# Optimization experiments

Hardware: AMD Instinct MI355X
Metric: run time of the kernel (lower is better)

The kernel has to match this reference:

```python
import jax, jax.numpy as jnp
import numpy as np


def setup_inputs() -> dict:
    key = jax.random.key(0)
    k1, k2, k3, k4 = jax.random.split(key, 4)
    B, S, D, Y = 8, 2048, 512, 8921
    # xavier_uniform scale for [Y, D] weights
    lim = float(np.sqrt(6.0 / (Y + D)))
    x = jax.random.normal(k1, (B, S, D), dtype=jnp.float32)
    U_w = jax.random.uniform(k2, (Y, D), minval=-lim, maxval=lim, dtype=jnp.float32)
    final_w = jax.random.uniform(k3, (Y, D), minval=-lim, maxval=lim, dtype=jnp.float32)
    final_b = jax.random.normal(k4, (Y,), dtype=jnp.float32) * 0.02
    return {"x": x, "U_w": U_w, "final_w": final_w, "final_b": final_b}


def reference(x, U_w, final_w, final_b):
    # att: [B, Y, S] = U_w @ x^T
    att = jnp.einsum("yd,bsd->bys", U_w, x)
    alpha = jax.nn.softmax(att, axis=2)          # softmax over sequence
    m = jnp.einsum("bys,bsd->byd", alpha, x)      # per-label context [B, Y, D]
    y = jnp.einsum("yd,byd->by", final_w, m) + final_b  # [B, Y]
    return y
```

## Files before the change

### kernel.cpp

```cpp
#include <hip/hip_runtime.h>
#include <hip/hip_bf16.h>

constexpr int B_ = 8;
constexpr int S_ = 2048;
constexpr int D_ = 512;
constexpr int Y_ = 8921;
constexpr int MT_ = 70;
constexpr int SG_ = 4;

typedef __attribute__((ext_vector_type(8))) __bf16 bf16x8;
typedef __attribute__((ext_vector_type(4))) float f32x4;

__device__ __forceinline__ int swz_el(int row, int ksel8) {
  return row * 64 + ((ksel8 ^ row) & 7) * 8;
}

__global__ __launch_bounds__(256) void cvtW(const float* __restrict__ U,
                                            const float* __restrict__ F,
                                            __hip_bfloat16* __restrict__ wsW) {
  const int c = blockIdx.x * 256 + threadIdx.x;
  const int tile = c >> 11;
  const int row = (c >> 3) & 255;
  const int cs = c & 7;
  const int mt = tile >> 3, kt = tile & 7;
  const int ch = cs ^ (row & 7);
  const int g = row >> 5, h = (row >> 4) & 1, w = row & 15;
  const int y = mt * 128 + g * 16 + w;
  float4 f0 = {0.f, 0.f, 0.f, 0.f}, f1 = {0.f, 0.f, 0.f, 0.f};
  if (y < Y_) {
    const float* src = (h ? F : U) + (size_t)y * D_ + kt * 64 + ch * 8;
    f0 = reinterpret_cast<const float4*>(src)[0];
    f1 = reinterpret_cast<const float4*>(src)[1];
  }
  bf16x8 v;
  v[0] = (__bf16)f0.x; v[1] = (__bf16)f0.y; v[2] = (__bf16)f0.z; v[3] = (__bf16)f0.w;
  v[4] = (__bf16)f1.x; v[5] = (__bf16)f1.y; v[6] = (__bf16)f1.z; v[7] = (__bf16)f1.w;
  *reinterpret_cast<bf16x8*>(wsW + (size_t)c * 8) = v;
}

__global__ __launch_bounds__(256) void cvtX(const float* __restrict__ x,
                                            __hip_bfloat16* __restrict__ wsX) {
  const int c = blockIdx.x * 256 + threadIdx.x;
  const int lane = c & 63;
  const int idx2 = (c >> 6) & 7;
  const int wn = (c >> 9) & 3;
  const int kt = (c >> 11) & 7;
  const int st = (c >> 14) & 7;
  const int b = (c >> 17) & 7;
  const int n = idx2 >> 1, kk = idx2 & 1;
  const int s = st * 256 + wn * 64 + n * 16 + (lane & 15);
  const int k = kt * 64 + kk * 32 + (lane >> 4) * 8;
  const float* src = x + ((size_t)b * S_ + s) * D_ + k;
  const float4 f0 = reinterpret_cast<const float4*>(src)[0];
  const float4 f1 = reinterpret_cast<const float4*>(src)[1];
  bf16x8 v;
  v[0] = (__bf16)f0.x; v[1] = (__bf16)f0.y; v[2] = (__bf16)f0.z; v[3] = (__bf16)f0.w;
  v[4] = (__bf16)f1.x; v[5] = (__bf16)f1.y; v[6] = (__bf16)f1.z; v[7] = (__bf16)f1.w;
  *reinterpret_cast<bf16x8*>(wsX + (size_t)c * 8) = v;
}

__global__ __launch_bounds__(256) void zeroLN(float* __restrict__ LN, int n) {
  const int i = blockIdx.x * 256 + threadIdx.x;
  if (i < n) LN[i] = 0.f;
}

__global__ __launch_bounds__(256) void combine(const float* __restrict__ Lg,
                                               const float* __restrict__ Ng,
                                               const float* __restrict__ fb,
                                               float* __restrict__ out) {
  const int y = blockIdx.x * 256 + threadIdx.x;
  const int b = blockIdx.y;
  if (y < Y_) out[(size_t)b * Y_ + y] = Ng[b * Y_ + y] / Lg[b * Y_ + y] + fb[y];
}

typedef const __attribute__((address_space(1))) void gv_t;
typedef __attribute__((address_space(3))) void lv_t;

__device__ __forceinline__ void gld_lds16(const void* g, void* l) {
  __builtin_amdgcn_global_load_lds((gv_t*)g, (lv_t*)l, 16, 0, 0);
}

__global__ __launch_bounds__(512, 2) void pool_main(
    const __hip_bfloat16* __restrict__ wsW, const __hip_bfloat16* __restrict__ wsX,
    float* __restrict__ Lg, float* __restrict__ Ng) {
  const int bid = blockIdx.x;
  const int b = bid & 7;
  const int r = bid >> 3;
  const int mt = r % MT_;
  const int sg = r / MT_;

  const int tid = threadIdx.x;
  const int lane = tid & 63;
  const int wid = tid >> 6;
  const int wm = wid >> 2;
  const int wn = wid & 3;
  const int l15 = lane & 15;
  const int l4 = lane >> 4;

  extern __shared__ __bf16 ldsA[];
  float* redLN = reinterpret_cast<float*>(ldsA + 4 * 16384);
  float* redL = redLN;
  float* redN = redLN + 128;

  if (tid < 256) redLN[tid] = 0.f;

  const __bf16* Wbase = (const __bf16*)wsW + (size_t)mt * 8 * 16384;
  const __bf16* xc = (const __bf16*)wsX +
      ((size_t)(b * 8 + sg * 2) * 8) * 16384 + wn * 4096 + lane * 8;

  f32x4 acc[8][4];
  bf16x8 X0[4], X1[4];

  auto stageA = [&](int wkt, int buf) {
    const char* src = (const char*)(Wbase + wkt * 16384) + wid * 4096 + lane * 16;
    char* dst = (char*)ldsA + buf * 32768 + wid * 4096;
#pragma unroll
    for (int i = 0; i < 4; ++i)
      gld_lds16(src + i * 1024, dst + i * 1024);
  };

  auto fold = [&]() {
#pragma unroll
    for (int g = 0; g < 4; ++g)
#pragma unroll
      for (int q = 0; q < 4; ++q) {
        float l = 0.f, nn = 0.f;
#pragma unroll
        for (int n = 0; n < 4; ++n) {
          const float e = __expf(acc[2 * g][n][q]);
          l += e;
          nn = fmaf(e, acc[2 * g + 1][n][q], nn);
        }
#pragma unroll
        for (int mask = 1; mask <= 8; mask <<= 1) {
          l += __shfl_xor(l, mask);
          nn += __shfl_xor(nn, mask);
        }
        if (l15 == 0) {
          const int yl = wm * 64 + g * 16 + (l4 << 2) + q;
          atomicAdd(&redL[yl], l);
          atomicAdd(&redN[yl], nn);
        }
      }
  };

  auto zacc = [&]() {
#pragma unroll
    for (int m = 0; m < 8; ++m)
#pragma unroll
      for (int n = 0; n < 4; ++n) acc[m][n] = (f32x4){0.f, 0.f, 0.f, 0.f};
  };

  stageA(0, 0);
  stageA(1, 1);
  stageA(2, 2);
#pragma unroll
  for (int n = 0; n < 4; ++n)
    X0[n] = *reinterpret_cast<const bf16x8*>(xc + n * 1024);
  asm volatile("s_waitcnt vmcnt(0) lgkmcnt(0)" ::: "memory");
  __builtin_amdgcn_s_barrier();
  __builtin_amdgcn_sched_barrier(0);
  zacc();

  for (int t = 0; t < 16; ++t) {
    if (t == 8) { fold(); zacc(); }
    const __bf16* A = ldsA + (t & 3) * 16384;

    {
      bf16x8 af[4];
#pragma unroll
      for (int j = 0; j < 4; ++j)
        af[j] = *reinterpret_cast<const bf16x8*>(
            &A[swz_el(wm * 128 + j * 16 + l15, l4)]);
#pragma unroll
      for (int n = 0; n < 4; ++n)
        X1[n] = *reinterpret_cast<const bf16x8*>(xc + n * 1024 + 512);
      if (t <= 12) stageA((t + 3) & 7, (t + 3) & 3);
      __builtin_amdgcn_s_barrier();
      __builtin_amdgcn_s_setprio(1);
#pragma unroll
      for (int j = 0; j < 4; ++j)
#pragma unroll
        for (int n = 0; n < 4; ++n)
          acc[j][n] = __builtin_amdgcn_mfma_f32_16x16x32_bf16(af[j], X0[n], acc[j][n], 0, 0, 0);
      __builtin_amdgcn_s_setprio(0);
      __builtin_amdgcn_s_barrier();
    }
    {
      bf16x8 af[4];
#pragma unroll
      for (int j = 0; j < 4; ++j)
        af[j] = *reinterpret_cast<const bf16x8*>(
            &A[swz_el(wm * 128 + (4 + j) * 16 + l15, l4)]);
      __builtin_amdgcn_s_barrier();
      __builtin_amdgcn_s_setprio(1);
#pragma unroll
      for (int j = 0; j < 4; ++j)
#pragma unroll
        for (int n = 0; n < 4; ++n)
          acc[4 + j][n] = __builtin_amdgcn_mfma_f32_16x16x32_bf16(af[j], X0[n], acc[4 + j][n], 0, 0, 0);
      __builtin_amdgcn_s_setprio(0);
      __builtin_amdgcn_s_barrier();
    }
    {
      bf16x8 af[4];
#pragma unroll
      for (int j = 0; j < 4; ++j)
        af[j] = *reinterpret_cast<const bf16x8*>(
            &A[swz_el(wm * 128 + j * 16 + l15, 4 + l4)]);
      if (t < 15) {
#pragma unroll
        for (int n = 0; n < 4; ++n)
          X0[n] = *reinterpret_cast<const bf16x8*>(xc + 16384 + n * 1024);
      }
      __builtin_amdgcn_s_barrier();
      __builtin_amdgcn_s_setprio(1);
#pragma unroll
      for (int j = 0; j < 4; ++j)
#pragma unroll
        for (int n = 0; n < 4; ++n)
          acc[j][n] = __builtin_amdgcn_mfma_f32_16x16x32_bf16(af[j], X1[n], acc[j][n], 0, 0, 0);
      __builtin_amdgcn_s_setprio(0);
      __builtin_amdgcn_s_barrier();
    }
    {
      bf16x8 af[4];
#pragma unroll
      for (int j = 0; j < 4; ++j)
        af[j] = *reinterpret_cast<const bf16x8*>(
            &A[swz_el(wm * 128 + (4 + j) * 16 + l15, 4 + l4)]);
      __builtin_amdgcn_s_barrier();
      __builtin_amdgcn_s_setprio(1);
#pragma unroll
      for (int j = 0; j < 4; ++j)
#pragma unroll
        for (int n = 0; n < 4; ++n)
          acc[4 + j][n] = __builtin_amdgcn_mfma_f32_16x16x32_bf16(af[j], X1[n], acc[4 + j][n], 0, 0, 0);
      __builtin_amdgcn_s_setprio(0);
      asm volatile("s_waitcnt vmcnt(8)" ::: "memory");
      __builtin_amdgcn_s_barrier();
      __builtin_amdgcn_sched_barrier(0);
    }
    xc += 16384;
  }
  fold();

  __syncthreads();
  if (tid < 128) {
    const int y = mt * 128 + tid;
    if (y < Y_) {
      atomicAdd(&Lg[(size_t)b * Y_ + y], redL[tid]);
      atomicAdd(&Ng[(size_t)b * Y_ + y], redN[tid]);
    }
  }
}

constexpr int FB_BY = 128, FB_BS = 64, FB_BK = 64;

__device__ __forceinline__ int fswz(int row, int k) {
  return row * FB_BK + ((((k >> 3) ^ row) & 7) << 3) + (k & 7);
}

template <int CHUNKS>
__device__ __forceinline__ void fb_stage(const float* __restrict__ gbase, int rstride,
                                         int maxrow, __bf16* lds, int tid) {
#pragma unroll
  for (int i = 0; i < CHUNKS / 256; ++i) {
    const int c = tid + 256 * i;
    const int row = c >> 3;
    const int ch = c & 7;
    float4 f0 = {0.f, 0.f, 0.f, 0.f}, f1 = {0.f, 0.f, 0.f, 0.f};
    if (row < maxrow) {
      const float4* p = reinterpret_cast<const float4*>(gbase + (size_t)row * rstride + ch * 8);
      f0 = p[0]; f1 = p[1];
    }
    bf16x8 v;
    v[0] = (__bf16)f0.x; v[1] = (__bf16)f0.y; v[2] = (__bf16)f0.z; v[3] = (__bf16)f0.w;
    v[4] = (__bf16)f1.x; v[5] = (__bf16)f1.y; v[6] = (__bf16)f1.z; v[7] = (__bf16)f1.w;
    *reinterpret_cast<bf16x8*>(&lds[fswz(row, ch * 8)]) = v;
  }
}

__global__ __launch_bounds__(256) void output_layer_fallback(
    const float* __restrict__ x, const float* __restrict__ Uw,
    const float* __restrict__ Fw, const float* __restrict__ fb,
    float* __restrict__ out) {
  const int b = blockIdx.y;
  const int y0 = blockIdx.x * FB_BY;
  const int tid = threadIdx.x;
  const int lane = tid & 63;
  const int w = tid >> 6;
  const int wm = (w >> 1) * 64, wn = (w & 1) * 32;
  __shared__ __bf16 sU[FB_BY * FB_BK], sF[FB_BY * FB_BK], sX[FB_BS * FB_BK];
  float Ls[4][4], Ns[4][4];
#pragma unroll
  for (int m = 0; m < 4; ++m)
#pragma unroll
    for (int q = 0; q < 4; ++q) { Ls[m][q] = 0.f; Ns[m][q] = 0.f; }
  const float* xb = x + (size_t)b * S_ * D_;
  const int umax = Y_ - y0;
  for (int s0 = 0; s0 < S_; s0 += FB_BS) {
    f32x4 accA[4][2] = {}, accP[4][2] = {};
    for (int k0 = 0; k0 < D_; k0 += FB_BK) {
      __syncthreads();
      fb_stage<FB_BY * 8>(Uw + (size_t)y0 * D_ + k0, D_, umax, sU, tid);
      fb_stage<FB_BY * 8>(Fw + (size_t)y0 * D_ + k0, D_, umax, sF, tid);
      fb_stage<FB_BS * 8>(xb + (size_t)s0 * D_ + k0, D_, FB_BS, sX, tid);
      __syncthreads();
#pragma unroll
      for (int kk = 0; kk < 2; ++kk) {
        const int kb = kk * 32 + (lane >> 4) * 8;
        bf16x8 bx[2];
#pragma unroll
        for (int n = 0; n < 2; ++n)
          bx[n] = *reinterpret_cast<const bf16x8*>(&sX[fswz(wn + n * 16 + (lane & 15), kb)]);
#pragma unroll
        for (int m = 0; m < 4; ++m) {
          const bf16x8 aU = *reinterpret_cast<const bf16x8*>(&sU[fswz(wm + m * 16 + (lane & 15), kb)]);
          const bf16x8 aF = *reinterpret_cast<const bf16x8*>(&sF[fswz(wm + m * 16 + (lane & 15), kb)]);
#pragma unroll
          for (int n = 0; n < 2; ++n) {
            accA[m][n] = __builtin_amdgcn_mfma_f32_16x16x32_bf16(aU, bx[n], accA[m][n], 0, 0, 0);
            accP[m][n] = __builtin_amdgcn_mfma_f32_16x16x32_bf16(aF, bx[n], accP[m][n], 0, 0, 0);
          }
        }
      }
    }
#pragma unroll
    for (int m = 0; m < 4; ++m)
#pragma unroll
      for (int n = 0; n < 2; ++n)
#pragma unroll
        for (int q = 0; q < 4; ++q) {
          const float e = __expf(accA[m][n][q]);
          Ls[m][q] += e;
          Ns[m][q] = fmaf(e, accP[m][n][q], Ns[m][q]);
        }
  }
  __syncthreads();
  float* redL = reinterpret_cast<float*>(sU);
  float* redN = reinterpret_cast<float*>(sF);
  for (int i = tid; i < FB_BY; i += 256) { redL[i] = 0.f; redN[i] = 0.f; }
  __syncthreads();
#pragma unroll
  for (int m = 0; m < 4; ++m)
#pragma unroll
    for (int q = 0; q < 4; ++q) {
      float l = Ls[m][q], nn = Ns[m][q];
#pragma unroll
      for (int mask = 1; mask <= 8; mask <<= 1) {
        l += __shfl_xor(l, mask);
        nn += __shfl_xor(nn, mask);
      }
      if ((lane & 15) == 0) {
        const int yl = wm + m * 16 + ((lane >> 4) << 2) + q;
        atomicAdd(&redL[yl], l);
        atomicAdd(&redN[yl], nn);
      }
    }
  __syncthreads();
  for (int i = tid; i < FB_BY; i += 256) {
    const int y = y0 + i;
    if (y < Y_) out[(size_t)b * Y_ + y] = redN[i] / redL[i] + fb[y];
  }
}

extern "C" void kernel_launch(void* const* d_in, const int* in_sizes, int n_in,
                              void* d_out, int out_size, void* d_ws,
                              size_t ws_size, hipStream_t stream) {
  const float* x = (const float*)d_in[0];
  const float* Uw = (const float*)d_in[1];
  const float* Fw = (const float*)d_in[2];
  const float* fb = (const float*)d_in[3];
  float* out = (float*)d_out;

  constexpr size_t W_EL = (size_t)MT_ * 8 * 16384;
  constexpr size_t X_EL = (size_t)B_ * 64 * 16384;
  constexpr size_t LN_FL = (size_t)2 * B_ * Y_;
  constexpr size_t WS_NEED = (W_EL + X_EL) * 2 + LN_FL * 4;
  constexpr int LDS_BYTES = 4 * 32768 + 1024;

  if (ws_size >= WS_NEED) {
    __hip_bfloat16* wsW = (__hip_bfloat16*)d_ws;
    __hip_bfloat16* wsX = wsW + W_EL;
    float* Lg = (float*)(wsX + X_EL);
    float* Ng = Lg + (size_t)B_ * Y_;

    cvtW<<<dim3((unsigned)(W_EL / 8 / 256)), dim3(256), 0, stream>>>(Uw, Fw, wsW);
    cvtX<<<dim3((unsigned)(X_EL / 8 / 256)), dim3(256), 0, stream>>>(x, wsX);
    zeroLN<<<dim3((unsigned)((LN_FL + 255) / 256)), dim3(256), 0, stream>>>(Lg, (int)LN_FL);

    hipFuncSetAttribute((const void*)pool_main,
                        hipFuncAttributeMaxDynamicSharedMemorySize, LDS_BYTES);
    pool_main<<<dim3(MT_ * B_ * SG_), dim3(512), LDS_BYTES, stream>>>(wsW, wsX, Lg, Ng);
    combine<<<dim3((Y_ + 255) / 256, B_), dim3(256), 0, stream>>>(Lg, Ng, fb, out);
  } else {
    output_layer_fallback<<<dim3(MT_, B_), dim3(256), 0, stream>>>(x, Uw, Fw, fb, out);
  }
}
```

Measured before the change: 399.7 us.

## Stage X tiles through LDS with double-buffered combined W/X loads

The X pre-conversion kernel now writes x in the same swizzled 256x64 tile layout used for the weights. The main pooling loop then stages both the W and X tiles into LDS with direct global-to-LDS loads, double-buffered, instead of a 4-deep W ring plus per-wave register loads of X. Each iteration now does one __syncthreads and two 32-deep MFMA phases that read X fragments from LDS, replacing four barrier-separated sub-phases. This simplifies synchronisation and shares X loads across waves, but the prefetch distance drops from three tiles to one and X now adds LDS read traffic.

```diff
diff --git a/kernel.cpp b/kernel.cpp
--- a/kernel.cpp
+++ b/kernel.cpp
@@ -41,16 +41,13 @@
 __global__ __launch_bounds__(256) void cvtX(const float* __restrict__ x,
                                             __hip_bfloat16* __restrict__ wsX) {
   const int c = blockIdx.x * 256 + threadIdx.x;
-  const int lane = c & 63;
-  const int idx2 = (c >> 6) & 7;
-  const int wn = (c >> 9) & 3;
-  const int kt = (c >> 11) & 7;
-  const int st = (c >> 14) & 7;
-  const int b = (c >> 17) & 7;
-  const int n = idx2 >> 1, kk = idx2 & 1;
-  const int s = st * 256 + wn * 64 + n * 16 + (lane & 15);
-  const int k = kt * 64 + kk * 32 + (lane >> 4) * 8;
-  const float* src = x + ((size_t)b * S_ + s) * D_ + k;
+  const int tile = c >> 11;
+  const int row = (c >> 3) & 255;
+  const int cs = c & 7;
+  const int b = tile >> 6, st = (tile >> 3) & 7, kt = tile & 7;
+  const int ch = cs ^ (row & 7);
+  const int s = st * 256 + row;
+  const float* src = x + ((size_t)b * S_ + s) * D_ + kt * 64 + ch * 8;
   const float4 f0 = reinterpret_cast<const float4*>(src)[0];
   const float4 f1 = reinterpret_cast<const float4*>(src)[1];
   bf16x8 v;
@@ -98,25 +95,26 @@
   const int l4 = lane >> 4;
 
   extern __shared__ __bf16 ldsA[];
-  float* redLN = reinterpret_cast<float*>(ldsA + 4 * 16384);
-  float* redL = redLN;
-  float* redN = redLN + 128;
-
-  if (tid < 256) redLN[tid] = 0.f;
+  float* redL = reinterpret_cast<float*>(ldsA + 65536);
+  float* redN = redL + 128;
+
+  if (tid < 256) redL[tid] = 0.f;
 
   const __bf16* Wbase = (const __bf16*)wsW + (size_t)mt * 8 * 16384;
-  const __bf16* xc = (const __bf16*)wsX +
-      ((size_t)(b * 8 + sg * 2) * 8) * 16384 + wn * 4096 + lane * 8;
+  const __bf16* Xbase = (const __bf16*)wsX + ((size_t)(b * 8 + sg * 2) * 8) * 16384;
 
   f32x4 acc[8][4];
-  bf16x8 X0[4], X1[4];
-
-  auto stageA = [&](int wkt, int buf) {
-    const char* src = (const char*)(Wbase + wkt * 16384) + wid * 4096 + lane * 16;
-    char* dst = (char*)ldsA + buf * 32768 + wid * 4096;
-#pragma unroll
-    for (int i = 0; i < 4; ++i)
-      gld_lds16(src + i * 1024, dst + i * 1024);
+
+  auto stageBoth = [&](int t1) {
+    const int par = t1 & 1;
+    const char* srcW = (const char*)(Wbase + (t1 & 7) * 16384) + wid * 4096 + lane * 16;
+    const char* srcX = (const char*)(Xbase + (size_t)t1 * 16384) + wid * 4096 + lane * 16;
+    char* dstW = (char*)ldsA + par * 32768 + wid * 4096;
+    char* dstX = (char*)ldsA + 65536 + par * 32768 + wid * 4096;
+#pragma unroll
+    for (int i = 0; i < 4; ++i) gld_lds16(srcW + i * 1024, dstW + i * 1024);
+#pragma unroll
+    for (int i = 0; i < 4; ++i) gld_lds16(srcX + i * 1024, dstX + i * 1024);
   };
 
   auto fold = [&]() {
@@ -151,97 +149,50 @@
       for (int n = 0; n < 4; ++n) acc[m][n] = (f32x4){0.f, 0.f, 0.f, 0.f};
   };
 
-  stageA(0, 0);
-  stageA(1, 1);
-  stageA(2, 2);
-#pragma unroll
-  for (int n = 0; n < 4; ++n)
-    X0[n] = *reinterpret_cast<const bf16x8*>(xc + n * 1024);
-  asm volatile("s_waitcnt vmcnt(0) lgkmcnt(0)" ::: "memory");
-  __builtin_amdgcn_s_barrier();
-  __builtin_amdgcn_sched_barrier(0);
+  stageBoth(0);
   zacc();
 
   for (int t = 0; t < 16; ++t) {
-    if (t == 8) { fold(); zacc(); }
-    const __bf16* A = ldsA + (t & 3) * 16384;
+    __syncthreads();
+    if (t < 15) stageBoth(t + 1);
+
+    const __bf16* A = ldsA + (t & 1) * 16384;
+    const __bf16* Xl = ldsA + 32768 + (t & 1) * 16384;
 
     {
-      bf16x8 af[4];
-#pragma unroll
-      for (int j = 0; j < 4; ++j)
-        af[j] = *reinterpret_cast<const bf16x8*>(
-            &A[swz_el(wm * 128 + j * 16 + l15, l4)]);
+      bf16x8 xf[4], af[8];
 #pragma unroll
       for (int n = 0; n < 4; ++n)
-        X1[n] = *reinterpret_cast<const bf16x8*>(xc + n * 1024 + 512);
-      if (t <= 12) stageA((t + 3) & 7, (t + 3) & 3);
-      __builtin_amdgcn_s_barrier();
+        xf[n] = *reinterpret_cast<const bf16x8*>(&Xl[swz_el(wn * 64 + n * 16 + l15, l4)]);
+#pragma unroll
+      for (int j = 0; j < 8; ++j)
+        af[j] = *reinterpret_cast<const bf16x8*>(&A[swz_el(wm * 128 + j * 16 + l15, l4)]);
       __builtin_amdgcn_s_setprio(1);
 #pragma unroll
-      for (int j = 0; j < 4; ++j)
+      for (int j = 0; j < 8; ++j)
 #pragma unroll
         for (int n = 0; n < 4; ++n)
-          acc[j][n] = __builtin_amdgcn_mfma_f32_16x16x32_bf16(af[j], X0[n], acc[j][n], 0, 0, 0);
+          acc[j][n] = __builtin_amdgcn_mfma_f32_16x16x32_bf16(af[j], xf[n], acc[j][n], 0, 0, 0);
       __builtin_amdgcn_s_setprio(0);
-      __builtin_amdgcn_s_barrier();
     }
     {
-      bf16x8 af[4];
-#pragma unroll
-      for (int j = 0; j < 4; ++j)
-        af[j] = *reinterpret_cast<const bf16x8*>(
-            &A[swz_el(wm * 128 + (4 + j) * 16 + l15, l4)]);
-      __builtin_amdgcn_s_barrier();
+      bf16x8 xf[4], af[8];
+#pragma unroll
+      for (int n = 0; n < 4; ++n)
+        xf[n] = *reinterpret_cast<const bf16x8*>(&Xl[swz_el(wn * 64 + n * 16 + l15, 4 + l4)]);
+#pragma unroll
+      for (int j = 0; j < 8; ++j)
+        af[j] = *reinterpret_cast<const bf16x8*>(&A[swz_el(wm * 128 + j * 16 + l15, 4 + l4)]);
       __builtin_amdgcn_s_setprio(1);
 #pragma unroll
-      for (int j = 0; j < 4; ++j)
+      for (int j = 0; j < 8; ++j)
 #pragma unroll
         for (int n = 0; n < 4; ++n)
-          acc[4 + j][n] = __builtin_amdgcn_mfma_f32_16x16x32_bf16(af[j], X0[n], acc[4 + j][n], 0, 0, 0);
+          acc[j][n] = __builtin_amdgcn_mfma_f32_16x16x32_bf16(af[j], xf[n], acc[j][n], 0, 0, 0);
       __builtin_amdgcn_s_setprio(0);
-      __builtin_amdgcn_s_barrier();
-    }
-    {
-      bf16x8 af[4];
-#pragma unroll
-      for (int j = 0; j < 4; ++j)
-        af[j] = *reinterpret_cast<const bf16x8*>(
-            &A[swz_el(wm * 128 + j * 16 + l15, 4 + l4)]);
-      if (t < 15) {
-#pragma unroll
-        for (int n = 0; n < 4; ++n)
-          X0[n] = *reinterpret_cast<const bf16x8*>(xc + 16384 + n * 1024);
-      }
-      __builtin_amdgcn_s_barrier();
-      __builtin_amdgcn_s_setprio(1);
-#pragma unroll
-      for (int j = 0; j < 4; ++j)
-#pragma unroll
-        for (int n = 0; n < 4; ++n)
-          acc[j][n] = __builtin_amdgcn_mfma_f32_16x16x32_bf16(af[j], X1[n], acc[j][n], 0, 0, 0);
-      __builtin_amdgcn_s_setprio(0);
-      __builtin_amdgcn_s_barrier();
-    }
-    {
-      bf16x8 af[4];
-#pragma unroll
-      for (int j = 0; j < 4; ++j)
-        af[j] = *reinterpret_cast<const bf16x8*>(
-            &A[swz_el(wm * 128 + (4 + j) * 16 + l15, 4 + l4)]);
-      __builtin_amdgcn_s_barrier();
-      __builtin_amdgcn_s_setprio(1);
-#pragma unroll
-      for (int j = 0; j < 4; ++j)
-#pragma unroll
-        for (int n = 0; n < 4; ++n)
-          acc[4 + j][n] = __builtin_amdgcn_mfma_f32_16x16x32_bf16(af[j], X1[n], acc[4 + j][n], 0, 0, 0);
-      __builtin_amdgcn_s_setprio(0);
-      asm volatile("s_waitcnt vmcnt(8)" ::: "memory");
-      __builtin_amdgcn_s_barrier();
-      __builtin_amdgcn_sched_barrier(0);
-    }
-    xc += 16384;
+    }
+
+    if (t == 7) { fold(); zacc(); }
   }
   fold();
 
```

Measured after the change: 347.2 us. -13.1%, faster.
